# Kernel optimization log

Measured on AMD Instinct MI355X. Metric: run time of the kernel, lower is better.

Reference implementation:

```python
import jax, jax.numpy as jnp
import numpy as np

F = 50          # num features
CARD = 10000    # cardinality per feature
D = 64          # factor_dim
A = 64          # attention_size
IU, JU = np.triu_indices(F, k=1)  # upper-triangular pair indices, P = F*(F-1)/2


def setup_inputs() -> dict:
    key = jax.random.key(0)
    ks = jax.random.split(key, 8)
    inputs = jax.random.randint(ks[0], (1024, F), 0, CARD, dtype=jnp.int32)
    emb_table = jax.random.normal(ks[1], (F * CARD, D), dtype=jnp.float32) * 0.05
    w_lin = jax.random.normal(ks[2], (F * CARD,), dtype=jnp.float32) * 0.05
    b_lin = jnp.zeros((1,), dtype=jnp.float32)
    W1 = jax.random.normal(ks[3], (D, A), dtype=jnp.float32) * (1.0 / np.sqrt(D))
    b1 = jnp.zeros((A,), dtype=jnp.float32)
    W2 = jax.random.normal(ks[4], (A, 1), dtype=jnp.float32) * (1.0 / np.sqrt(A))
    b2 = jnp.zeros((1,), dtype=jnp.float32)
    return {"inputs": inputs, "emb_table": emb_table, "w_lin": w_lin,
            "b_lin": b_lin, "W1": W1, "b1": b1, "W2": W2, "b2": b2}


def reference(inputs, emb_table, w_lin, b_lin, W1, b1, W2, b2):
    # Per-feature tables are stacked into one flat table; offset indices per feature.
    flat_idx = inputs + (jnp.arange(F, dtype=jnp.int32) * CARD)[None, :]  # [B, F]
    line_out = jnp.sum(w_lin[flat_idx], axis=1, keepdims=True) + b_lin    # [B, 1]
    factor = emb_table[flat_idx]                                          # [B, F, D]
    # Upper-triangular pairwise element-wise products (i < j), P = F(F-1)/2
    inter = factor[:, IU, :] * factor[:, JU, :]                           # [B, P, D]
    # Attention: Dense(A) -> ReLU -> Dense(1) -> Softmax over pairs
    h = jax.nn.relu(jnp.einsum('bpd,da->bpa', inter, W1) + b1)            # [B, P, A]
    logits = jnp.einsum('bpa,ao->bpo', h, W2) + b2                        # [B, P, 1]
    scores = jax.nn.softmax(logits, axis=1)                               # [B, P, 1]
    pooled = jnp.sum(inter, axis=-1, keepdims=True)                       # [B, P, 1]
    return line_out + jnp.sum(pooled * scores, axis=1)                    # [B, 1]
```

## Files before the change

### kernel.cpp

```cpp
#include <hip/hip_runtime.h>
#include <math.h>

#define FN 50
#define CARD 10000
#define NP 1225
#define NTILE 77
#define NPAD (NTILE*16)
#define FSTRIDE 72

typedef _Float16 half8 __attribute__((ext_vector_type(8)));
typedef __fp16 half2t __attribute__((ext_vector_type(2)));
typedef __fp16 half4t __attribute__((ext_vector_type(4)));
typedef float floatx4 __attribute__((ext_vector_type(4)));

static __device__ __forceinline__ half2t h2max0(half2t v) {
  half2t r;
  r[0] = v[0] > (__fp16)0 ? v[0] : (__fp16)0;
  r[1] = v[1] > (__fp16)0 ? v[1] : (__fp16)0;
  return r;
}
static __device__ __forceinline__ float hdot2(half2t a, half2t b, float c) {
#if __has_builtin(__builtin_amdgcn_fdot2)
  return __builtin_amdgcn_fdot2(a, b, c, false);
#else
  return c + (float)a[0]*(float)b[0] + (float)a[1]*(float)b[1];
#endif
}

__global__ __launch_bounds__(256, 4)
void afm_kernel(const int* __restrict__ inp,
                const float* __restrict__ emb,
                const float* __restrict__ wlin,
                const float* __restrict__ blin,
                const float* __restrict__ W1,
                const float* __restrict__ b1,
                const float* __restrict__ W2,
                const float* __restrict__ b2,
                float* __restrict__ out)
{
  __shared__ __align__(16) _Float16 s_fac[FN][FSTRIDE];
  __shared__ __align__(16) _Float16 s_w1[512 * 8];
  __shared__ __align__(16) unsigned s_pij[NPAD];
  __shared__ float s_wl[FN];
  __shared__ float s_red[8];

  const int tid  = threadIdx.x;
  const int b    = blockIdx.x;
  const int lane = tid & 63;
  const int wave = tid >> 6;
  const int c    = lane & 15;
  const int kq   = lane >> 4;

  for (int p = tid; p < NPAD; p += 256) {
    int pp = p < NP ? p : NP - 1;
    int i = (int)((99.0f - sqrtf(9801.0f - 8.0f * (float)pp)) * 0.5f);
    if (i < 0) i = 0;
    while ((i + 1) * (98 - i) / 2 <= pp) ++i;
    while (i > 0 && i * (99 - i) / 2 > pp) --i;
    int j = pp - i * (99 - i) / 2 + i + 1;
    s_pij[p] = (unsigned)(i * (FSTRIDE * 2)) | ((unsigned)(j * (FSTRIDE * 2)) << 16);
  }

  const int* inprow = inp + b * FN;
  for (int idx = tid; idx < FN * 16; idx += 256) {
    int f = idx >> 4, q = idx & 15;
    int flat = inprow[f] + f * CARD;
    floatx4 v = ((const floatx4*)emb)[(long)flat * 16 + q];
    half2t lo = __builtin_amdgcn_cvt_pkrtz(v[0], v[1]);
    half2t hi = __builtin_amdgcn_cvt_pkrtz(v[2], v[3]);
    half4t pk = {lo[0], lo[1], hi[0], hi[1]};
    *(half4t*)&s_fac[f][q * 4] = pk;
  }
  if (tid < FN) {
    int flat = inprow[tid] + tid * CARD;
    s_wl[tid] = wlin[flat];
  }

  for (int ch = tid; ch < 512; ch += 256) {
    int ks = ch >> 8, mt = (ch >> 6) & 3, ln = ch & 63;
    int cc = ln & 15, kk = ln >> 4;
    __fp16 tmp[8];
#pragma unroll
    for (int j = 0; j < 4; ++j) {
      float x = W1[(ks * 32 + kk * 8 + 2 * j)     * 64 + mt * 16 + cc];
      float y = W1[(ks * 32 + kk * 8 + 2 * j + 1) * 64 + mt * 16 + cc];
      half2t hw = __builtin_amdgcn_cvt_pkrtz(x, y);
      tmp[2 * j] = hw[0]; tmp[2 * j + 1] = hw[1];
    }
    *(half8*)&s_w1[ch * 8] = *(const half8*)tmp;
  }

  floatx4 bias[4];
  half2t w2h[4][2];
#pragma unroll
  for (int mt = 0; mt < 4; ++mt) {
    bias[mt] = ((const floatx4*)b1)[mt * 4 + kq];
    floatx4 wv = ((const floatx4*)W2)[mt * 4 + kq];
    w2h[mt][0] = __builtin_amdgcn_cvt_pkrtz(wv[0], wv[1]);
    w2h[mt][1] = __builtin_amdgcn_cvt_pkrtz(wv[2], wv[3]);
  }
  _Float16 onev = (c == 0) ? (_Float16)1 : (_Float16)0;
  half8 onesf = {onev, onev, onev, onev, onev, onev, onev, onev};

  __syncthreads();

#define LDW1(ks, mt) (*(const half8*)&s_w1[(((ks) * 4 + (mt)) * 64 + lane) * 8])
  const char* fbase = (const char*)&s_fac[0][0];
  const int koff = kq * 16;
  float se = 0.f, spe = 0.f;
  {
    int t = wave;
    int pcur = t * 16 + c;
    unsigned po_cur = s_pij[pcur];
    int pn1 = (t + 4) * 16 + c; if (pn1 > NPAD - 1) pn1 = NPAD - 1;
    unsigned po_nx = s_pij[pn1];
    int offi = (int)(po_cur & 0xffffu) + koff;
    int offj = (int)(po_cur >> 16) + koff;
    half8 cvi0 = *(const half8*)(fbase + offi);
    half8 cvj0 = *(const half8*)(fbase + offj);
    half8 cvi1 = *(const half8*)(fbase + offi + 64);
    half8 cvj1 = *(const half8*)(fbase + offj + 64);

    while (true) {
      int pn2 = (t + 8) * 16 + c; if (pn2 > NPAD - 1) pn2 = NPAD - 1;
      unsigned po_n2 = s_pij[pn2];

      half8 pr0 = cvi0 * cvj0;
      half8 pr1 = cvi1 * cvj1;

      floatx4 acc[4];
#pragma unroll
      for (int mt = 0; mt < 4; ++mt) {
        acc[mt] = __builtin_amdgcn_mfma_f32_16x16x32_f16(LDW1(0, mt), pr0, bias[mt], 0, 0, 0);
        acc[mt] = __builtin_amdgcn_mfma_f32_16x16x32_f16(LDW1(1, mt), pr1, acc[mt], 0, 0, 0);
      }
      floatx4 accp = __builtin_amdgcn_mfma_f32_16x16x32_f16(onesf, pr0, (floatx4){0.f,0.f,0.f,0.f}, 0, 0, 0);
      accp = __builtin_amdgcn_mfma_f32_16x16x32_f16(onesf, pr1, accp, 0, 0, 0);

      int offi_n = (int)(po_nx & 0xffffu) + koff;
      int offj_n = (int)(po_nx >> 16) + koff;
      cvi0 = *(const half8*)(fbase + offi_n);
      cvj0 = *(const half8*)(fbase + offj_n);
      cvi1 = *(const half8*)(fbase + offi_n + 64);
      cvj1 = *(const half8*)(fbase + offj_n + 64);

      float lg = 0.f;
#pragma unroll
      for (int mt = 0; mt < 4; ++mt) {
        half2t h0 = __builtin_amdgcn_cvt_pkrtz(acc[mt][0], acc[mt][1]);
        half2t h1 = __builtin_amdgcn_cvt_pkrtz(acc[mt][2], acc[mt][3]);
        h0 = h2max0(h0);
        h1 = h2max0(h1);
        lg = hdot2(h0, w2h[mt][0], lg);
        lg = hdot2(h1, w2h[mt][1], lg);
      }
      lg += __shfl_xor(lg, 16, 64);
      lg += __shfl_xor(lg, 32, 64);
      float e = __expf(lg);
      if (kq == 0 && pcur < NP) {
        se  += e;
        spe += e * accp[0];
      }

      t += 4;
      if (t >= NTILE) break;
      pcur = t * 16 + c;
      po_nx = po_n2;
    }
  }
#undef LDW1

#pragma unroll
  for (int o = 1; o <= 8; o <<= 1) {
    se  += __shfl_xor(se, o, 64);
    spe += __shfl_xor(spe, o, 64);
  }
  if (lane == 0) { s_red[wave] = se; s_red[4 + wave] = spe; }
  __syncthreads();
  if (tid == 0) {
    float line = blin[0];
#pragma unroll
    for (int f = 0; f < FN; ++f) line += s_wl[f];
    float SE  = s_red[0] + s_red[1] + s_red[2] + s_red[3];
    float SPE = s_red[4] + s_red[5] + s_red[6] + s_red[7];
    out[b] = line + SPE / SE;
  }
}

extern "C" void kernel_launch(void* const* d_in, const int* in_sizes, int n_in,
                              void* d_out, int out_size, void* d_ws, size_t ws_size,
                              hipStream_t stream) {
  const int*   inp  = (const int*)d_in[0];
  const float* emb  = (const float*)d_in[1];
  const float* wlin = (const float*)d_in[2];
  const float* blin = (const float*)d_in[3];
  const float* W1   = (const float*)d_in[4];
  const float* b1   = (const float*)d_in[5];
  const float* W2   = (const float*)d_in[6];
  const float* b2   = (const float*)d_in[7];
  float* outp = (float*)d_out;
  const int B = in_sizes[0] / FN;
  afm_kernel<<<B, 256, 0, stream>>>(inp, emb, wlin, blin, W1, b1, W2, b2, outp);
}
```

Before: 24.02 us.

## Switch attention matmul to 32x32x16 MFMA tiles and pool with dot2

Each wave now handles 32 pairs per tile and computes the attention hidden layer with 32x32x16 f16 MFMAs instead of 16x16x32 ones, with W1 repacked in LDS to match the new operand layout. The pairwise-sum pooling is done with packed fp16 dot2 instructions rather than an extra MFMA against a ones vector. b1 is added in fp16 after conversion instead of seeding the accumulator. This aims to cut MFMA instruction count and loop iterations, but it drops the previous one-tile-ahead prefetch of factor vectors, adds padded tail work, and slightly changes bias rounding.

```diff
diff --git a/kernel.cpp b/kernel.cpp
--- a/kernel.cpp
+++ b/kernel.cpp
@@ -4,14 +4,15 @@
 #define FN 50
 #define CARD 10000
 #define NP 1225
-#define NTILE 77
-#define NPAD (NTILE*16)
+#define NPAD 1232
+#define NT32 39
 #define FSTRIDE 72
 
 typedef _Float16 half8 __attribute__((ext_vector_type(8)));
 typedef __fp16 half2t __attribute__((ext_vector_type(2)));
 typedef __fp16 half4t __attribute__((ext_vector_type(4)));
 typedef float floatx4 __attribute__((ext_vector_type(4)));
+typedef float floatx16 __attribute__((ext_vector_type(16)));
 
 static __device__ __forceinline__ half2t h2max0(half2t v) {
   half2t r;
@@ -42,14 +43,14 @@
   __shared__ __align__(16) _Float16 s_w1[512 * 8];
   __shared__ __align__(16) unsigned s_pij[NPAD];
   __shared__ float s_wl[FN];
-  __shared__ float s_red[8];
+  __shared__ float s_red[16];
 
   const int tid  = threadIdx.x;
   const int b    = blockIdx.x;
   const int lane = tid & 63;
   const int wave = tid >> 6;
-  const int c    = lane & 15;
-  const int kq   = lane >> 4;
+  const int n32  = lane & 31;
+  const int hi   = lane >> 5;
 
   for (int p = tid; p < NPAD; p += 256) {
     int pp = p < NP ? p : NP - 1;
@@ -67,8 +68,8 @@
     int flat = inprow[f] + f * CARD;
     floatx4 v = ((const floatx4*)emb)[(long)flat * 16 + q];
     half2t lo = __builtin_amdgcn_cvt_pkrtz(v[0], v[1]);
-    half2t hi = __builtin_amdgcn_cvt_pkrtz(v[2], v[3]);
-    half4t pk = {lo[0], lo[1], hi[0], hi[1]};
+    half2t hi2 = __builtin_amdgcn_cvt_pkrtz(v[2], v[3]);
+    half4t pk = {lo[0], lo[1], hi2[0], hi2[1]};
     *(half4t*)&s_fac[f][q * 4] = pk;
   }
   if (tid < FN) {
@@ -77,112 +78,110 @@
   }
 
   for (int ch = tid; ch < 512; ch += 256) {
-    int ks = ch >> 8, mt = (ch >> 6) & 3, ln = ch & 63;
-    int cc = ln & 15, kk = ln >> 4;
+    int mt = ch >> 8, ks = (ch >> 6) & 3, ln = ch & 63;
+    int a = mt * 32 + (ln & 31);
+    int kb = ks * 16 + (ln >> 5) * 8;
     __fp16 tmp[8];
 #pragma unroll
     for (int j = 0; j < 4; ++j) {
-      float x = W1[(ks * 32 + kk * 8 + 2 * j)     * 64 + mt * 16 + cc];
-      float y = W1[(ks * 32 + kk * 8 + 2 * j + 1) * 64 + mt * 16 + cc];
-      half2t hw = __builtin_amdgcn_cvt_pkrtz(x, y);
+      half2t hw = __builtin_amdgcn_cvt_pkrtz(W1[(kb + 2 * j) * 64 + a],
+                                             W1[(kb + 2 * j + 1) * 64 + a]);
       tmp[2 * j] = hw[0]; tmp[2 * j + 1] = hw[1];
     }
     *(half8*)&s_w1[ch * 8] = *(const half8*)tmp;
   }
 
-  floatx4 bias[4];
-  half2t w2h[4][2];
-#pragma unroll
-  for (int mt = 0; mt < 4; ++mt) {
-    bias[mt] = ((const floatx4*)b1)[mt * 4 + kq];
-    floatx4 wv = ((const floatx4*)W2)[mt * 4 + kq];
-    w2h[mt][0] = __builtin_amdgcn_cvt_pkrtz(wv[0], wv[1]);
-    w2h[mt][1] = __builtin_amdgcn_cvt_pkrtz(wv[2], wv[3]);
-  }
-  _Float16 onev = (c == 0) ? (_Float16)1 : (_Float16)0;
-  half8 onesf = {onev, onev, onev, onev, onev, onev, onev, onev};
+  half2t b1h[2][4][2], w2h[2][4][2];
+#pragma unroll
+  for (int mt = 0; mt < 2; ++mt)
+#pragma unroll
+    for (int q = 0; q < 4; ++q) {
+      floatx4 bv = *(const floatx4*)&b1[mt * 32 + q * 8 + 4 * hi];
+      floatx4 wv = *(const floatx4*)&W2[mt * 32 + q * 8 + 4 * hi];
+      b1h[mt][q][0] = __builtin_amdgcn_cvt_pkrtz(bv[0], bv[1]);
+      b1h[mt][q][1] = __builtin_amdgcn_cvt_pkrtz(bv[2], bv[3]);
+      w2h[mt][q][0] = __builtin_amdgcn_cvt_pkrtz(wv[0], wv[1]);
+      w2h[mt][q][1] = __builtin_amdgcn_cvt_pkrtz(wv[2], wv[3]);
+    }
+  const half2t one2 = {(__fp16)1, (__fp16)1};
 
   __syncthreads();
 
-#define LDW1(ks, mt) (*(const half8*)&s_w1[(((ks) * 4 + (mt)) * 64 + lane) * 8])
+#define LDW1(mt, ks) (*(const half8*)&s_w1[(((mt) * 4 + (ks)) * 64 + lane) * 8])
   const char* fbase = (const char*)&s_fac[0][0];
-  const int koff = kq * 16;
+  const int hib = hi * 16;
   float se = 0.f, spe = 0.f;
   {
     int t = wave;
-    int pcur = t * 16 + c;
-    unsigned po_cur = s_pij[pcur];
-    int pn1 = (t + 4) * 16 + c; if (pn1 > NPAD - 1) pn1 = NPAD - 1;
+    int p = t * 32 + n32;
+    unsigned po = s_pij[p < NPAD ? p : NPAD - 1];
+    int pn1 = (t + 4) * 32 + n32; if (pn1 > NPAD - 1) pn1 = NPAD - 1;
     unsigned po_nx = s_pij[pn1];
-    int offi = (int)(po_cur & 0xffffu) + koff;
-    int offj = (int)(po_cur >> 16) + koff;
-    half8 cvi0 = *(const half8*)(fbase + offi);
-    half8 cvj0 = *(const half8*)(fbase + offj);
-    half8 cvi1 = *(const half8*)(fbase + offi + 64);
-    half8 cvj1 = *(const half8*)(fbase + offj + 64);
 
     while (true) {
-      int pn2 = (t + 8) * 16 + c; if (pn2 > NPAD - 1) pn2 = NPAD - 1;
+      int pn2 = (t + 8) * 32 + n32; if (pn2 > NPAD - 1) pn2 = NPAD - 1;
       unsigned po_n2 = s_pij[pn2];
 
-      half8 pr0 = cvi0 * cvj0;
-      half8 pr1 = cvi1 * cvj1;
-
-      floatx4 acc[4];
-#pragma unroll
-      for (int mt = 0; mt < 4; ++mt) {
-        acc[mt] = __builtin_amdgcn_mfma_f32_16x16x32_f16(LDW1(0, mt), pr0, bias[mt], 0, 0, 0);
-        acc[mt] = __builtin_amdgcn_mfma_f32_16x16x32_f16(LDW1(1, mt), pr1, acc[mt], 0, 0, 0);
+      int offi = (int)(po & 0xffffu) + hib;
+      int offj = (int)(po >> 16) + hib;
+      half8 pr[4];
+#pragma unroll
+      for (int ks = 0; ks < 4; ++ks) {
+        half8 fi = *(const half8*)(fbase + offi + ks * 32);
+        half8 fj = *(const half8*)(fbase + offj + ks * 32);
+        pr[ks] = fi * fj;
       }
-      floatx4 accp = __builtin_amdgcn_mfma_f32_16x16x32_f16(onesf, pr0, (floatx4){0.f,0.f,0.f,0.f}, 0, 0, 0);
-      accp = __builtin_amdgcn_mfma_f32_16x16x32_f16(onesf, pr1, accp, 0, 0, 0);
-
-      int offi_n = (int)(po_nx & 0xffffu) + koff;
-      int offj_n = (int)(po_nx >> 16) + koff;
-      cvi0 = *(const half8*)(fbase + offi_n);
-      cvj0 = *(const half8*)(fbase + offj_n);
-      cvi1 = *(const half8*)(fbase + offi_n + 64);
-      cvj1 = *(const half8*)(fbase + offj_n + 64);
 
       float lg = 0.f;
 #pragma unroll
-      for (int mt = 0; mt < 4; ++mt) {
-        half2t h0 = __builtin_amdgcn_cvt_pkrtz(acc[mt][0], acc[mt][1]);
-        half2t h1 = __builtin_amdgcn_cvt_pkrtz(acc[mt][2], acc[mt][3]);
-        h0 = h2max0(h0);
-        h1 = h2max0(h1);
-        lg = hdot2(h0, w2h[mt][0], lg);
-        lg = hdot2(h1, w2h[mt][1], lg);
+      for (int mt = 0; mt < 2; ++mt) {
+        floatx16 acc = {0.f};
+#pragma unroll
+        for (int ks = 0; ks < 4; ++ks)
+          acc = __builtin_amdgcn_mfma_f32_32x32x16_f16(LDW1(mt, ks), pr[ks], acc, 0, 0, 0);
+#pragma unroll
+        for (int q = 0; q < 4; ++q) {
+          half2t h0 = __builtin_amdgcn_cvt_pkrtz(acc[q * 4 + 0], acc[q * 4 + 1]);
+          half2t h1 = __builtin_amdgcn_cvt_pkrtz(acc[q * 4 + 2], acc[q * 4 + 3]);
+          h0 = h2max0(h0 + b1h[mt][q][0]);
+          h1 = h2max0(h1 + b1h[mt][q][1]);
+          lg = hdot2(h0, w2h[mt][q][0], lg);
+          lg = hdot2(h1, w2h[mt][q][1], lg);
+        }
       }
-      lg += __shfl_xor(lg, 16, 64);
-      lg += __shfl_xor(lg, 32, 64);
+      float pool = 0.f;
+#pragma unroll
+      for (int ks = 0; ks < 4; ++ks) {
+        const half2t* pp2 = (const half2t*)&pr[ks];
+#pragma unroll
+        for (int q = 0; q < 4; ++q) pool = hdot2(pp2[q], one2, pool);
+      }
+      lg   += __shfl_xor(lg, 32, 64);
+      pool += __shfl_xor(pool, 32, 64);
       float e = __expf(lg);
-      if (kq == 0 && pcur < NP) {
-        se  += e;
-        spe += e * accp[0];
-      }
+      if (hi == 0 && p < NP) { se += e; spe += e * pool; }
 
       t += 4;
-      if (t >= NTILE) break;
-      pcur = t * 16 + c;
-      po_nx = po_n2;
+      if (t >= NT32) break;
+      p = t * 32 + n32;
+      po = po_nx; po_nx = po_n2;
     }
   }
 #undef LDW1
 
 #pragma unroll
-  for (int o = 1; o <= 8; o <<= 1) {
+  for (int o = 1; o <= 32; o <<= 1) {
     se  += __shfl_xor(se, o, 64);
     spe += __shfl_xor(spe, o, 64);
   }
-  if (lane == 0) { s_red[wave] = se; s_red[4 + wave] = spe; }
+  if (lane == 0) { s_red[wave] = se; s_red[8 + wave] = spe; }
   __syncthreads();
   if (tid == 0) {
     float line = blin[0];
 #pragma unroll
     for (int f = 0; f < FN; ++f) line += s_wl[f];
-    float SE  = s_red[0] + s_red[1] + s_red[2] + s_red[3];
-    float SPE = s_red[4] + s_red[5] + s_red[6] + s_red[7];
+    float SE  = s_red[0] + s_red[1] + s_red[2]  + s_red[3];
+    float SPE = s_red[8] + s_red[9] + s_red[10] + s_red[11];
     out[b] = line + SPE / SE;
   }
 }
```

Result: slower. 25.18 us (+4.8%).

## Split each batch row across two blocks with atomic cross-block softmax reduction

Applied to the files above, without the earlier changes.

Each batch row is now processed by two blocks, each covering half of the pair tiles. The blocks combine their partial softmax sums through global atomics and a completion counter, and the last block writes the output. The pooled sum over D moves from a ones-matrix MFMA to packed fp16 dot products. The b1 bias is now added in fp16 after conversion instead of seeding the MFMA accumulator. This doubles grid parallelism for the small batch and raises occupancy hints. In exchange, each block repeats the embedding gather and W1 staging, and the change adds a memset launch and atomic traffic.

```diff
diff --git a/kernel.cpp b/kernel.cpp
--- a/kernel.cpp
+++ b/kernel.cpp
@@ -27,7 +27,7 @@
 #endif
 }
 
-__global__ __launch_bounds__(256, 4)
+__global__ __launch_bounds__(256, 6)
 void afm_kernel(const int* __restrict__ inp,
                 const float* __restrict__ emb,
                 const float* __restrict__ wlin,
@@ -35,8 +35,10 @@
                 const float* __restrict__ W1,
                 const float* __restrict__ b1,
                 const float* __restrict__ W2,
-                const float* __restrict__ b2,
-                float* __restrict__ out)
+                float* __restrict__ out,
+                float* __restrict__ wse,
+                float* __restrict__ wspe,
+                unsigned* __restrict__ wcnt)
 {
   __shared__ __align__(16) _Float16 s_fac[FN][FSTRIDE];
   __shared__ __align__(16) _Float16 s_w1[512 * 8];
@@ -45,7 +47,8 @@
   __shared__ float s_red[8];
 
   const int tid  = threadIdx.x;
-  const int b    = blockIdx.x;
+  const int r    = blockIdx.x >> 1;
+  const int h    = blockIdx.x & 1;
   const int lane = tid & 63;
   const int wave = tid >> 6;
   const int c    = lane & 15;
@@ -61,7 +64,7 @@
     s_pij[p] = (unsigned)(i * (FSTRIDE * 2)) | ((unsigned)(j * (FSTRIDE * 2)) << 16);
   }
 
-  const int* inprow = inp + b * FN;
+  const int* inprow = inp + r * FN;
   for (int idx = tid; idx < FN * 16; idx += 256) {
     int f = idx >> 4, q = idx & 15;
     int flat = inprow[f] + f * CARD;
@@ -90,17 +93,17 @@
     *(half8*)&s_w1[ch * 8] = *(const half8*)tmp;
   }
 
-  floatx4 bias[4];
-  half2t w2h[4][2];
+  half2t b1h[4][2], w2h[4][2];
 #pragma unroll
   for (int mt = 0; mt < 4; ++mt) {
-    bias[mt] = ((const floatx4*)b1)[mt * 4 + kq];
+    floatx4 bv = ((const floatx4*)b1)[mt * 4 + kq];
     floatx4 wv = ((const floatx4*)W2)[mt * 4 + kq];
+    b1h[mt][0] = __builtin_amdgcn_cvt_pkrtz(bv[0], bv[1]);
+    b1h[mt][1] = __builtin_amdgcn_cvt_pkrtz(bv[2], bv[3]);
     w2h[mt][0] = __builtin_amdgcn_cvt_pkrtz(wv[0], wv[1]);
     w2h[mt][1] = __builtin_amdgcn_cvt_pkrtz(wv[2], wv[3]);
   }
-  _Float16 onev = (c == 0) ? (_Float16)1 : (_Float16)0;
-  half8 onesf = {onev, onev, onev, onev, onev, onev, onev, onev};
+  const half2t one2 = {(__fp16)1, (__fp16)1};
 
   __syncthreads();
 
@@ -109,21 +112,21 @@
   const int koff = kq * 16;
   float se = 0.f, spe = 0.f;
   {
-    int t = wave;
+    int t = h * 4 + wave;
     int pcur = t * 16 + c;
-    unsigned po_cur = s_pij[pcur];
-    int pn1 = (t + 4) * 16 + c; if (pn1 > NPAD - 1) pn1 = NPAD - 1;
-    unsigned po_nx = s_pij[pn1];
-    int offi = (int)(po_cur & 0xffffu) + koff;
-    int offj = (int)(po_cur >> 16) + koff;
+    unsigned po = s_pij[pcur];
+    int i1 = (t + 8) * 16 + c; if (i1 > NPAD - 1) i1 = NPAD - 1;
+    unsigned po_nx = s_pij[i1];
+    int offi = (int)(po & 0xffffu) + koff;
+    int offj = (int)(po >> 16) + koff;
     half8 cvi0 = *(const half8*)(fbase + offi);
     half8 cvj0 = *(const half8*)(fbase + offj);
     half8 cvi1 = *(const half8*)(fbase + offi + 64);
     half8 cvj1 = *(const half8*)(fbase + offj + 64);
 
     while (true) {
-      int pn2 = (t + 8) * 16 + c; if (pn2 > NPAD - 1) pn2 = NPAD - 1;
-      unsigned po_n2 = s_pij[pn2];
+      int i2 = (t + 16) * 16 + c; if (i2 > NPAD - 1) i2 = NPAD - 1;
+      unsigned po_n2 = s_pij[i2];
 
       half8 pr0 = cvi0 * cvj0;
       half8 pr1 = cvi1 * cvj1;
@@ -131,11 +134,20 @@
       floatx4 acc[4];
 #pragma unroll
       for (int mt = 0; mt < 4; ++mt) {
-        acc[mt] = __builtin_amdgcn_mfma_f32_16x16x32_f16(LDW1(0, mt), pr0, bias[mt], 0, 0, 0);
+        acc[mt] = __builtin_amdgcn_mfma_f32_16x16x32_f16(LDW1(0, mt), pr0, (floatx4){0.f,0.f,0.f,0.f}, 0, 0, 0);
         acc[mt] = __builtin_amdgcn_mfma_f32_16x16x32_f16(LDW1(1, mt), pr1, acc[mt], 0, 0, 0);
       }
-      floatx4 accp = __builtin_amdgcn_mfma_f32_16x16x32_f16(onesf, pr0, (floatx4){0.f,0.f,0.f,0.f}, 0, 0, 0);
-      accp = __builtin_amdgcn_mfma_f32_16x16x32_f16(onesf, pr1, accp, 0, 0, 0);
+
+      float pool = 0.f;
+      {
+        const half2t* pp0 = (const half2t*)&pr0;
+        const half2t* pp1 = (const half2t*)&pr1;
+#pragma unroll
+        for (int q = 0; q < 4; ++q) {
+          pool = hdot2(pp0[q], one2, pool);
+          pool = hdot2(pp1[q], one2, pool);
+        }
+      }
 
       int offi_n = (int)(po_nx & 0xffffu) + koff;
       int offj_n = (int)(po_nx >> 16) + koff;
@@ -149,20 +161,19 @@
       for (int mt = 0; mt < 4; ++mt) {
         half2t h0 = __builtin_amdgcn_cvt_pkrtz(acc[mt][0], acc[mt][1]);
         half2t h1 = __builtin_amdgcn_cvt_pkrtz(acc[mt][2], acc[mt][3]);
-        h0 = h2max0(h0);
-        h1 = h2max0(h1);
+        h0 = h2max0(h0 + b1h[mt][0]);
+        h1 = h2max0(h1 + b1h[mt][1]);
         lg = hdot2(h0, w2h[mt][0], lg);
         lg = hdot2(h1, w2h[mt][1], lg);
       }
-      lg += __shfl_xor(lg, 16, 64);
-      lg += __shfl_xor(lg, 32, 64);
+      lg   += __shfl_xor(lg, 16, 64);
+      lg   += __shfl_xor(lg, 32, 64);
+      pool += __shfl_xor(pool, 16, 64);
+      pool += __shfl_xor(pool, 32, 64);
       float e = __expf(lg);
-      if (kq == 0 && pcur < NP) {
-        se  += e;
-        spe += e * accp[0];
-      }
-
-      t += 4;
+      if (kq == 0 && pcur < NP) { se += e; spe += e * pool; }
+
+      t += 8;
       if (t >= NTILE) break;
       pcur = t * 16 + c;
       po_nx = po_n2;
@@ -178,12 +189,20 @@
   if (lane == 0) { s_red[wave] = se; s_red[4 + wave] = spe; }
   __syncthreads();
   if (tid == 0) {
-    float line = blin[0];
-#pragma unroll
-    for (int f = 0; f < FN; ++f) line += s_wl[f];
-    float SE  = s_red[0] + s_red[1] + s_red[2] + s_red[3];
-    float SPE = s_red[4] + s_red[5] + s_red[6] + s_red[7];
-    out[b] = line + SPE / SE;
+    float se_b  = s_red[0] + s_red[1] + s_red[2] + s_red[3];
+    float spe_b = s_red[4] + s_red[5] + s_red[6] + s_red[7];
+    atomicAdd(&wse[r], se_b);
+    atomicAdd(&wspe[r], spe_b);
+    __threadfence();
+    unsigned old = atomicAdd(&wcnt[r], 1u);
+    if (old == 1) {
+      float SE  = atomicAdd(&wse[r], 0.0f);
+      float SPE = atomicAdd(&wspe[r], 0.0f);
+      float line = blin[0];
+#pragma unroll
+      for (int f = 0; f < FN; ++f) line += s_wl[f];
+      out[r] = line + SPE / SE;
+    }
   }
 }
 
@@ -197,8 +216,14 @@
   const float* W1   = (const float*)d_in[4];
   const float* b1   = (const float*)d_in[5];
   const float* W2   = (const float*)d_in[6];
-  const float* b2   = (const float*)d_in[7];
   float* outp = (float*)d_out;
   const int B = in_sizes[0] / FN;
-  afm_kernel<<<B, 256, 0, stream>>>(inp, emb, wlin, blin, W1, b1, W2, b2, outp);
-}
+
+  float*    wse  = (float*)d_ws;
+  float*    wspe = wse + B;
+  unsigned* wcnt = (unsigned*)(wspe + B);
+  hipMemsetAsync(d_ws, 0, (size_t)B * 12, stream);
+
+  afm_kernel<<<2 * B, 256, 0, stream>>>(inp, emb, wlin, blin, W1, b1, W2,
+                                        outp, wse, wspe, wcnt);
+}
```

After: 89.77 us. 274% more time.
